# Kernel optimization log

Hardware: AMD Instinct MI355X
Metric: run time of the kernel (lower is better)

Reference implementation:

```python
import jax, jax.numpy as jnp
import numpy as np

N = 30000
E_RAND = 480000
NFEAT = 512
NHID = 64
NHEADS = 8
NCLASS = 500
ALPHA = 0.2


def setup_inputs() -> dict:
    key = jax.random.key(0)
    ks = jax.random.split(key, 8)
    features = jax.random.normal(ks[0], (N, NFEAT), dtype=jnp.float32)
    src = jax.random.randint(ks[1], (E_RAND,), 0, N, dtype=jnp.int32)
    dst = jax.random.randint(ks[2], (E_RAND,), 0, N, dtype=jnp.int32)
    loop = jnp.arange(N, dtype=jnp.int32)
    edge_index = jnp.stack([jnp.concatenate([src, loop]), jnp.concatenate([dst, loop])])  # [2, E]
    # xavier-normal-ish scaling keeps exp(-leakyrelu(.)) in a sane range
    W = jax.random.normal(ks[3], (NHEADS, NFEAT, NHID), dtype=jnp.float32) * (1.414 * np.sqrt(2.0 / (NFEAT + NHID)))
    a = jax.random.normal(ks[4], (NHEADS, 2 * NHID), dtype=jnp.float32) * (1.414 * np.sqrt(2.0 / (1 + 2 * NHID)))
    out_W = jax.random.normal(ks[5], (NHID * NHEADS, NCLASS), dtype=jnp.float32) * (1.414 * np.sqrt(2.0 / (NHID * NHEADS + NCLASS)))
    out_a = jax.random.normal(ks[6], (2 * NCLASS,), dtype=jnp.float32) * (1.414 * np.sqrt(2.0 / (1 + 2 * NCLASS)))
    return {"features": features, "edge_index": edge_index, "W": W, "a": a, "out_W": out_W, "out_a": out_a}


def _sp_gat_layer(x, W, a, src, dst, concat):
    # h = x @ W  -> [N, F']
    h = x @ W
    f = h.shape[1]
    n = x.shape[0]
    # a . cat(h[src], h[dst]) == (h @ a[:f])[src] + (h @ a[f:])[dst]  (avoids [E, 2F'] concat)
    s_src = h @ a[:f]
    s_dst = h @ a[f:]
    logits = s_src[src] + s_dst[dst]                      # [E]
    edge_e = jnp.exp(-jax.nn.leaky_relu(logits, negative_slope=ALPHA))
    # special_spmm(edge, edge_e, [N,N], ones)  -> per-row sum of attention values
    e_rowsum = jax.ops.segment_sum(edge_e, src, num_segments=n)        # [N]
    # special_spmm(edge, edge_e, [N,N], h)     -> attention-weighted neighbor sum
    h_prime = jax.ops.segment_sum(edge_e[:, None] * h[dst], src, num_segments=n)  # [N, F']
    h_prime = h_prime / e_rowsum[:, None]
    return jax.nn.elu(h_prime) if concat else h_prime


def reference(features, edge_index, W, a, out_W, out_a):
    src, dst = edge_index[0], edge_index[1]
    # multi-head sparse GAT (concat=True per head), python loop over fixed small head count
    heads = [_sp_gat_layer(features, W[i], a[i], src, dst, concat=True) for i in range(W.shape[0])]
    x = jnp.concatenate(heads, axis=1)                    # [N, nhid*nheads]
    out = jax.nn.elu(_sp_gat_layer(x, out_W, out_a, src, dst, concat=False))  # [N, nclass]
    return out
```

## Files before the change

### kernel.cpp

```cpp
#include <hip/hip_runtime.h>
#include <math.h>

typedef __attribute__((ext_vector_type(8))) short short8;
typedef __attribute__((ext_vector_type(4))) float f32x4;

#define NFEAT 512
#define HID_ALL 512
#define NCLASS 500
#define ALPHA 0.2f
#define BM 128
#define BN 128

__device__ __forceinline__ ushort f32_to_bf16(float f) {
    union { float f; unsigned u; } v; v.f = f;
    unsigned u = v.u;
    unsigned r = (u + 0x7FFFu + ((u >> 16) & 1u)) >> 16;
    return (ushort)r;
}
__device__ __forceinline__ void unpack8(uint4 u, float* f) {
    f[0] = __uint_as_float(u.x << 16);
    f[1] = __uint_as_float(u.x & 0xFFFF0000u);
    f[2] = __uint_as_float(u.y << 16);
    f[3] = __uint_as_float(u.y & 0xFFFF0000u);
    f[4] = __uint_as_float(u.z << 16);
    f[5] = __uint_as_float(u.z & 0xFFFF0000u);
    f[6] = __uint_as_float(u.w << 16);
    f[7] = __uint_as_float(u.w & 0xFFFF0000u);
}
__device__ __forceinline__ float att_w(float lg) {
    return __expf(lg > 0.f ? -lg : -ALPHA * lg);
}
__device__ __forceinline__ void gload16(const void* g, void* l) {
    __builtin_amdgcn_global_load_lds(
        (const __attribute__((address_space(1))) unsigned int*)g,
        (__attribute__((address_space(3))) unsigned int*)l,
        16, 0, 0);
}

__global__ void prep_kernel(const float* __restrict__ oa, float* __restrict__ oas,
                            float* __restrict__ oad,
                            int* __restrict__ cnt, int* __restrict__ cur,
                            float* __restrict__ s2, float* __restrict__ d2, int N) {
    int idx = blockIdx.x * blockDim.x + threadIdx.x;
    if (idx < 512) {
        oas[idx] = (idx < NCLASS) ? oa[idx] : 0.f;
        oad[idx] = (idx < NCLASS) ? oa[NCLASS + idx] : 0.f;
    }
    if (idx < N) { cnt[idx] = 0; cur[idx] = 0; s2[idx] = 0.f; d2[idx] = 0.f; }
}

__global__ __launch_bounds__(256) void transpose_w1_kernel(const float* __restrict__ W,
                                                           ushort* __restrict__ WT) {
    __shared__ float tile[64][65];
    int head = blockIdx.x >> 3;
    int f0 = (blockIdx.x & 7) << 6;
    int tx = threadIdx.x & 63, tyb = threadIdx.x >> 6;
    const float* Wh = W + ((size_t)head << 15);
#pragma unroll
    for (int r = 0; r < 16; r++) {
        int ty = (tyb << 4) + r;
        tile[ty][tx] = Wh[(size_t)(f0 + ty) * 64 + tx];
    }
    __syncthreads();
#pragma unroll
    for (int r = 0; r < 16; r++) {
        int ty = (tyb << 4) + r;
        WT[(size_t)((head << 6) + ty) * 512 + f0 + tx] = f32_to_bf16(tile[tx][ty]);
    }
}

__global__ __launch_bounds__(256) void transpose_w2_kernel(const float* __restrict__ oW,
                                                           ushort* __restrict__ WT) {
    __shared__ float tile[64][65];
    int f0 = (blockIdx.x >> 3) << 6;
    int c0 = (blockIdx.x & 7) << 6;
    int tx = threadIdx.x & 63, tyb = threadIdx.x >> 6;
#pragma unroll
    for (int r = 0; r < 16; r++) {
        int ty = (tyb << 4) + r;
        int c = c0 + tx;
        tile[ty][tx] = (c < NCLASS) ? oW[(size_t)(f0 + ty) * NCLASS + c] : 0.f;
    }
    __syncthreads();
#pragma unroll
    for (int r = 0; r < 16; r++) {
        int ty = (tyb << 4) + r;
        WT[(size_t)(c0 + ty) * 512 + f0 + tx] = f32_to_bf16(tile[tx][ty]);
    }
}

__global__ void cast_feat_kernel(const float* __restrict__ in, ushort* __restrict__ out, int n4) {
    int stride = gridDim.x * blockDim.x;
    for (int i = blockIdx.x * blockDim.x + threadIdx.x; i < n4; i += stride) {
        float4 v = reinterpret_cast<const float4*>(in)[i];
        ushort4 o;
        o.x = f32_to_bf16(v.x); o.y = f32_to_bf16(v.y);
        o.z = f32_to_bf16(v.z); o.w = f32_to_bf16(v.w);
        reinterpret_cast<ushort4*>(out)[i] = o;
    }
}

__global__ void edge_count_kernel(const int* __restrict__ src, int* __restrict__ cnt, int E) {
    int e = blockIdx.x * blockDim.x + threadIdx.x;
    if (e < E) atomicAdd(&cnt[src[e]], 1);
}

__global__ __launch_bounds__(1024) void scan_kernel(const int* __restrict__ cnt,
                                                    int* __restrict__ rowptr, int n) {
    __shared__ int part[1024];
    int t = threadIdx.x;
    int chunk = (n + 1023) >> 10;
    int beg = t * chunk;
    int end = beg + chunk; if (end > n) end = n;
    int s = 0;
    for (int i = beg; i < end; i++) s += cnt[i];
    part[t] = s;
    __syncthreads();
    for (int off = 1; off < 1024; off <<= 1) {
        int v = part[t];
        int add = (t >= off) ? part[t - off] : 0;
        __syncthreads();
        part[t] = v + add;
        __syncthreads();
    }
    int base = (t > 0) ? part[t - 1] : 0;
    for (int i = beg; i < end; i++) { rowptr[i] = base; base += cnt[i]; }
    if (t == 1023) rowptr[n] = part[1023];
}

__global__ void scatter_kernel(const int* __restrict__ src, const int* __restrict__ dst,
                               const int* __restrict__ rowptr, int* __restrict__ cur,
                               int* __restrict__ colidx, int E) {
    int e = blockIdx.x * blockDim.x + threadIdx.x;
    if (e >= E) return;
    int s = src[e];
    int p = rowptr[s] + atomicAdd(&cur[s], 1);
    colidx[p] = dst[e];
}

template <int MODE>
__global__ __launch_bounds__(256) void gemm_fused_kernel(const ushort* __restrict__ A,
                                                         const ushort* __restrict__ Bt,
                                                         ushort* __restrict__ C,
                                                         const float* __restrict__ av,
                                                         const float* __restrict__ av2,
                                                         float* __restrict__ sv,
                                                         float* __restrict__ dv,
                                                         int M) {
    __shared__ ushort As[BM * 64];
    __shared__ ushort Bs[BN * 64];
    int m0 = blockIdx.x * BM;
    int n0 = blockIdx.y * BN;
    int t = threadIdx.x;
    int lane = t & 63, wid = t >> 6;
    int wr = wid >> 1, wc = wid & 1;
    int g = lane >> 4, r15 = lane & 15;
    int srow = lane >> 3;
    int schunk = lane & 7;
    f32x4 acc[4][4] = {};
    for (int k0 = 0; k0 < 512; k0 += 64) {
        __syncthreads();
#pragma unroll
        for (int j = 0; j < 4; j++) {
            int rb = j * 32 + wid * 8;
            int r = rb + srow;
            int ca = (schunk ^ (srow & 7)) << 3;
            int rowA = m0 + r; if (rowA >= M) rowA = M - 1;
            gload16(&A[(size_t)rowA * 512 + k0 + ca], &As[rb * 64]);
            int rowB = n0 + r;
            gload16(&Bt[(size_t)rowB * 512 + k0 + ca], &Bs[rb * 64]);
        }
        __syncthreads();
#pragma unroll
        for (int kk = 0; kk < 2; kk++) {
            int coff = ((kk * 4 + g) ^ (r15 & 7)) << 3;
            short8 af[4], bfr[4];
#pragma unroll
            for (int mi = 0; mi < 4; mi++)
                af[mi] = *reinterpret_cast<const short8*>(&As[((wr << 6) + mi * 16 + r15) * 64 + coff]);
#pragma unroll
            for (int ni = 0; ni < 4; ni++)
                bfr[ni] = *reinterpret_cast<const short8*>(&Bs[((wc << 6) + ni * 16 + r15) * 64 + coff]);
#pragma unroll
            for (int mi = 0; mi < 4; mi++)
#pragma unroll
                for (int ni = 0; ni < 4; ni++)
                    acc[mi][ni] = __builtin_amdgcn_mfma_f32_16x16x32_bf16(af[mi], bfr[ni], acc[mi][ni], 0, 0, 0);
        }
    }
    int fr = g << 2;
    int col = r15;
#pragma unroll
    for (int mi = 0; mi < 4; mi++)
#pragma unroll
        for (int ni = 0; ni < 4; ni++)
#pragma unroll
            for (int r = 0; r < 4; r++) {
                int grow = m0 + (wr << 6) + mi * 16 + fr + r;
                if (grow < M) {
                    int gcol = n0 + (wc << 6) + ni * 16 + col;
                    C[(size_t)grow * 512 + gcol] = f32_to_bf16(acc[mi][ni][r]);
                }
            }
    float ws[4], wd[4];
    int h = (n0 >> 6) + wc;
#pragma unroll
    for (int ni = 0; ni < 4; ni++) {
        if (MODE == 0) {
            int k = ni * 16 + col;
            ws[ni] = av[(h << 7) + k];
            wd[ni] = av[(h << 7) + 64 + k];
        } else {
            int gcol = n0 + (wc << 6) + ni * 16 + col;
            ws[ni] = av[gcol];
            wd[ni] = av2[gcol];
        }
    }
#pragma unroll
    for (int mi = 0; mi < 4; mi++)
#pragma unroll
        for (int r = 0; r < 4; r++) {
            float ps = 0.f, pd = 0.f;
#pragma unroll
            for (int ni = 0; ni < 4; ni++) {
                float v = acc[mi][ni][r];
                ps += v * ws[ni];
                pd += v * wd[ni];
            }
#pragma unroll
            for (int off = 1; off < 16; off <<= 1) {
                ps += __shfl_xor(ps, off);
                pd += __shfl_xor(pd, off);
            }
            int grow = m0 + (wr << 6) + mi * 16 + fr + r;
            if (col == 0 && grow < M) {
                if (MODE == 0) {
                    sv[(grow << 3) + h] = ps;
                    dv[(grow << 3) + h] = pd;
                } else {
                    atomicAdd(&sv[grow], ps);
                    atomicAdd(&dv[grow], pd);
                }
            }
        }
}

#define LOAD4_1(C0,C1,C2,C3,G0,G1,G2,G3,U0,U1,U2,U3,ii)                                  \
    C0 = colidx[ii]; C1 = colidx[ii + 1]; C2 = colidx[ii + 2]; C3 = colidx[ii + 3];      \
    G0 = d1[(C0 << 3) + h]; G1 = d1[(C1 << 3) + h];                                      \
    G2 = d1[(C2 << 3) + h]; G3 = d1[(C3 << 3) + h];                                      \
    U0 = *reinterpret_cast<const uint4*>(&h1[(size_t)C0 * 512 + lane * 8]);              \
    U1 = *reinterpret_cast<const uint4*>(&h1[(size_t)C1 * 512 + lane * 8]);              \
    U2 = *reinterpret_cast<const uint4*>(&h1[(size_t)C2 * 512 + lane * 8]);              \
    U3 = *reinterpret_cast<const uint4*>(&h1[(size_t)C3 * 512 + lane * 8]);

#define CONS4(G0,G1,G2,G3,U0,U1,U2,U3)                                                   \
    {                                                                                    \
        float w0 = att_w(sn + G0), w1 = att_w(sn + G1);                                  \
        float w2 = att_w(sn + G2), w3 = att_w(sn + G3);                                  \
        rsum += (w0 + w1) + (w2 + w3);                                                   \
        float f[8];                                                                      \
        unpack8(U0, f);                                                                  \
        _Pragma("unroll") for (int q = 0; q < 8; q++) acc[q] += w0 * f[q];               \
        unpack8(U1, f);                                                                  \
        _Pragma("unroll") for (int q = 0; q < 8; q++) acc[q] += w1 * f[q];               \
        unpack8(U2, f);                                                                  \
        _Pragma("unroll") for (int q = 0; q < 8; q++) acc[q] += w2 * f[q];               \
        unpack8(U3, f);                                                                  \
        _Pragma("unroll") for (int q = 0; q < 8; q++) acc[q] += w3 * f[q];               \
    }

__global__ __launch_bounds__(256) void agg1_kernel(const ushort* __restrict__ h1,
                                                   const float* __restrict__ s1,
                                                   const float* __restrict__ d1,
                                                   const int* __restrict__ rowptr,
                                                   const int* __restrict__ colidx,
                                                   ushort* __restrict__ x, int N) {
    int lane = threadIdx.x & 63;
    int n = (blockIdx.x << 2) + (threadIdx.x >> 6);
    if (n >= N) return;
    int h = lane >> 3;
    float sn = s1[(n << 3) + h];
    float acc[8] = {0.f, 0.f, 0.f, 0.f, 0.f, 0.f, 0.f, 0.f};
    float rsum = 0.f;
    int beg = rowptr[n], end = rowptr[n + 1];
    int i = beg;
    {
        int ac0, ac1, ac2, ac3, bc0, bc1, bc2, bc3;
        float ag0, ag1, ag2, ag3, bg0, bg1, bg2, bg3;
        uint4 au0, au1, au2, au3, bu0, bu1, bu2, bu3;
        if (i + 4 <= end) {
            LOAD4_1(ac0, ac1, ac2, ac3, ag0, ag1, ag2, ag3, au0, au1, au2, au3, i);
            i += 4;
            while (i + 4 <= end) {
                LOAD4_1(bc0, bc1, bc2, bc3, bg0, bg1, bg2, bg3, bu0, bu1, bu2, bu3, i);
                i += 4;
                CONS4(ag0, ag1, ag2, ag3, au0, au1, au2, au3);
                if (i + 4 <= end) {
                    LOAD4_1(ac0, ac1, ac2, ac3, ag0, ag1, ag2, ag3, au0, au1, au2, au3, i);
                    i += 4;
                    CONS4(bg0, bg1, bg2, bg3, bu0, bu1, bu2, bu3);
                } else {
                    CONS4(bg0, bg1, bg2, bg3, bu0, bu1, bu2, bu3);
                    goto tail1;
                }
            }
            CONS4(ag0, ag1, ag2, ag3, au0, au1, au2, au3);
        }
    }
tail1:
    for (; i < end; i++) {
        int dv = colidx[i];
        float w = att_w(sn + d1[(dv << 3) + h]);
        rsum += w;
        uint4 u = *reinterpret_cast<const uint4*>(&h1[(size_t)dv * 512 + lane * 8]);
        float f[8]; unpack8(u, f);
#pragma unroll
        for (int q = 0; q < 8; q++) acc[q] += w * f[q];
    }
    float inv = 1.f / rsum;
    uint ov[4];
#pragma unroll
    for (int p = 0; p < 4; p++) {
        float v0 = acc[2 * p] * inv;     v0 = v0 > 0.f ? v0 : __expf(v0) - 1.f;
        float v1 = acc[2 * p + 1] * inv; v1 = v1 > 0.f ? v1 : __expf(v1) - 1.f;
        ov[p] = (uint)f32_to_bf16(v0) | ((uint)f32_to_bf16(v1) << 16);
    }
    uint4 o; o.x = ov[0]; o.y = ov[1]; o.z = ov[2]; o.w = ov[3];
    *reinterpret_cast<uint4*>(&x[(size_t)n * 512 + lane * 8]) = o;
}

#define LOAD4_2(C0,C1,C2,C3,G0,G1,G2,G3,U0,U1,U2,U3,ii)                                  \
    C0 = colidx[ii]; C1 = colidx[ii + 1]; C2 = colidx[ii + 2]; C3 = colidx[ii + 3];      \
    G0 = d2[C0]; G1 = d2[C1]; G2 = d2[C2]; G3 = d2[C3];                                  \
    U0 = *reinterpret_cast<const uint4*>(&h2[(size_t)C0 * 512 + c0]);                    \
    U1 = *reinterpret_cast<const uint4*>(&h2[(size_t)C1 * 512 + c0]);                    \
    U2 = *reinterpret_cast<const uint4*>(&h2[(size_t)C2 * 512 + c0]);                    \
    U3 = *reinterpret_cast<const uint4*>(&h2[(size_t)C3 * 512 + c0]);

__global__ __launch_bounds__(256) void agg2_kernel(const ushort* __restrict__ h2,
                                                   const float* __restrict__ s2,
                                                   const float* __restrict__ d2,
                                                   const int* __restrict__ rowptr,
                                                   const int* __restrict__ colidx,
                                                   float* __restrict__ out, int N) {
    int lane = threadIdx.x & 63;
    int n = (blockIdx.x << 2) + (threadIdx.x >> 6);
    if (n >= N) return;
    int c0 = lane * 8;
    float sn = s2[n];
    float acc[8] = {0.f, 0.f, 0.f, 0.f, 0.f, 0.f, 0.f, 0.f};
    float rsum = 0.f;
    int beg = rowptr[n], end = rowptr[n + 1];
    int i = beg;
    {
        int ac0, ac1, ac2, ac3, bc0, bc1, bc2, bc3;
        float ag0, ag1, ag2, ag3, bg0, bg1, bg2, bg3;
        uint4 au0, au1, au2, au3, bu0, bu1, bu2, bu3;
        if (i + 4 <= end) {
            LOAD4_2(ac0, ac1, ac2, ac3, ag0, ag1, ag2, ag3, au0, au1, au2, au3, i);
            i += 4;
            while (i + 4 <= end) {
                LOAD4_2(bc0, bc1, bc2, bc3, bg0, bg1, bg2, bg3, bu0, bu1, bu2, bu3, i);
                i += 4;
                CONS4(ag0, ag1, ag2, ag3, au0, au1, au2, au3);
                if (i + 4 <= end) {
                    LOAD4_2(ac0, ac1, ac2, ac3, ag0, ag1, ag2, ag3, au0, au1, au2, au3, i);
                    i += 4;
                    CONS4(bg0, bg1, bg2, bg3, bu0, bu1, bu2, bu3);
                } else {
                    CONS4(bg0, bg1, bg2, bg3, bu0, bu1, bu2, bu3);
                    goto tail2;
                }
            }
            CONS4(ag0, ag1, ag2, ag3, au0, au1, au2, au3);
        }
    }
tail2:
    for (; i < end; i++) {
        int dv = colidx[i];
        float w = att_w(sn + d2[dv]);
        rsum += w;
        uint4 u = *reinterpret_cast<const uint4*>(&h2[(size_t)dv * 512 + c0]);
        float f[8]; unpack8(u, f);
#pragma unroll
        for (int q = 0; q < 8; q++) acc[q] += w * f[q];
    }
    float inv = 1.f / rsum;
#pragma unroll
    for (int q = 0; q < 8; q++) {
        int c = c0 + q;
        if (c < NCLASS) {
            float v = acc[q] * inv;
            v = v > 0.f ? v : __expf(v) - 1.f;
            out[(size_t)n * NCLASS + c] = v;
        }
    }
}

extern "C" void kernel_launch(void* const* d_in, const int* in_sizes, int n_in,
                              void* d_out, int out_size, void* d_ws, size_t ws_size,
                              hipStream_t stream) {
    const float* features = (const float*)d_in[0];
    const int* edge_index = (const int*)d_in[1];
    const float* W = (const float*)d_in[2];
    const float* a = (const float*)d_in[3];
    const float* out_W = (const float*)d_in[4];
    const float* out_a = (const float*)d_in[5];
    float* out = (float*)d_out;

    int N = in_sizes[0] / NFEAT;
    int E = in_sizes[1] / 2;
    const int* src = edge_index;
    const int* dst = edge_index + E;

    char* base = (char*)d_ws;
    size_t off = 0;
    auto alloc = [&](size_t bytes) -> char* {
        char* r = base + off;
        off += (bytes + 255) & ~(size_t)255;
        return r;
    };
    ushort* featb = (ushort*)alloc((size_t)N * 512 * 2);
    ushort* h1b   = (ushort*)alloc((size_t)N * 512 * 2);
    ushort* xb    = (ushort*)alloc((size_t)N * 512 * 2);
    ushort* h2b   = featb;
    ushort* w1t   = (ushort*)alloc(512 * 512 * 2);
    ushort* w2t   = (ushort*)alloc(512 * 512 * 2);
    float* s1 = (float*)alloc((size_t)N * 8 * 4);
    float* d1 = (float*)alloc((size_t)N * 8 * 4);
    float* s2 = (float*)alloc((size_t)N * 4);
    float* d2 = (float*)alloc((size_t)N * 4);
    float* oas = (float*)alloc(512 * 4);
    float* oad = (float*)alloc(512 * 4);
    int* rowptr = (int*)alloc((size_t)(N + 1) * 4);
    int* colidx = (int*)alloc((size_t)E * 4);
    int* cnt = (int*)alloc((size_t)N * 4);
    int* cur = (int*)alloc((size_t)N * 4);
    if (off > ws_size) return;

    prep_kernel<<<(N + 255) / 256, 256, 0, stream>>>(out_a, oas, oad, cnt, cur, s2, d2, N);
    transpose_w1_kernel<<<64, 256, 0, stream>>>(W, w1t);
    transpose_w2_kernel<<<64, 256, 0, stream>>>(out_W, w2t);
    cast_feat_kernel<<<2048, 256, 0, stream>>>(features, featb, N * 512 / 4);
    edge_count_kernel<<<(E + 255) / 256, 256, 0, stream>>>(src, cnt, E);
    scan_kernel<<<1, 1024, 0, stream>>>(cnt, rowptr, N);
    scatter_kernel<<<(E + 255) / 256, 256, 0, stream>>>(src, dst, rowptr, cur, colidx, E);

    dim3 gemm_grid((N + BM - 1) / BM, HID_ALL / BN);
    gemm_fused_kernel<0><<<gemm_grid, 256, 0, stream>>>(featb, w1t, h1b, a, nullptr, s1, d1, N);
    agg1_kernel<<<(N + 3) / 4, 256, 0, stream>>>(h1b, s1, d1, rowptr, colidx, xb, N);
    gemm_fused_kernel<1><<<gemm_grid, 256, 0, stream>>>(xb, w2t, h2b, oas, oad, s2, d2, N);
    agg2_kernel<<<(N + 3) / 4, 256, 0, stream>>>(h2b, s2, d2, rowptr, colidx, out, N);
}
```

Before: 345.4 us.

## Fuse feature bf16 cast into first GEMM and merge setup kernels

The first GEMM now reads fp32 features directly and converts them to bf16 while staging into LDS, removing the separate cast kernel and its bf16 buffer. The weight transposes and the zero/prep work are merged into a single launch, and the scan's partial sums use int4 loads. This saves one full read/write pass over the features and some launch overhead. In exchange the GEMM's A tile is loaded through registers at double the byte width instead of asynchronously into LDS.

```diff
diff --git a/kernel.cpp b/kernel.cpp
--- a/kernel.cpp
+++ b/kernel.cpp
@@ -37,66 +37,58 @@
         16, 0, 0);
 }
 
-__global__ void prep_kernel(const float* __restrict__ oa, float* __restrict__ oas,
-                            float* __restrict__ oad,
-                            int* __restrict__ cnt, int* __restrict__ cur,
-                            float* __restrict__ s2, float* __restrict__ d2, int N) {
-    int idx = blockIdx.x * blockDim.x + threadIdx.x;
-    if (idx < 512) {
-        oas[idx] = (idx < NCLASS) ? oa[idx] : 0.f;
-        oad[idx] = (idx < NCLASS) ? oa[NCLASS + idx] : 0.f;
-    }
-    if (idx < N) { cnt[idx] = 0; cur[idx] = 0; s2[idx] = 0.f; d2[idx] = 0.f; }
-}
-
-__global__ __launch_bounds__(256) void transpose_w1_kernel(const float* __restrict__ W,
-                                                           ushort* __restrict__ WT) {
+__global__ __launch_bounds__(256) void setup_kernel(const float* __restrict__ W,
+                                                    ushort* __restrict__ W1T,
+                                                    const float* __restrict__ oW,
+                                                    ushort* __restrict__ W2T,
+                                                    const float* __restrict__ oa,
+                                                    float* __restrict__ oas,
+                                                    float* __restrict__ oad,
+                                                    int* __restrict__ cnt, int* __restrict__ cur,
+                                                    float* __restrict__ s2, float* __restrict__ d2,
+                                                    int N) {
     __shared__ float tile[64][65];
-    int head = blockIdx.x >> 3;
-    int f0 = (blockIdx.x & 7) << 6;
-    int tx = threadIdx.x & 63, tyb = threadIdx.x >> 6;
-    const float* Wh = W + ((size_t)head << 15);
-#pragma unroll
-    for (int r = 0; r < 16; r++) {
-        int ty = (tyb << 4) + r;
-        tile[ty][tx] = Wh[(size_t)(f0 + ty) * 64 + tx];
-    }
-    __syncthreads();
-#pragma unroll
-    for (int r = 0; r < 16; r++) {
-        int ty = (tyb << 4) + r;
-        WT[(size_t)((head << 6) + ty) * 512 + f0 + tx] = f32_to_bf16(tile[tx][ty]);
-    }
-}
-
-__global__ __launch_bounds__(256) void transpose_w2_kernel(const float* __restrict__ oW,
-                                                           ushort* __restrict__ WT) {
-    __shared__ float tile[64][65];
-    int f0 = (blockIdx.x >> 3) << 6;
-    int c0 = (blockIdx.x & 7) << 6;
-    int tx = threadIdx.x & 63, tyb = threadIdx.x >> 6;
-#pragma unroll
-    for (int r = 0; r < 16; r++) {
-        int ty = (tyb << 4) + r;
-        int c = c0 + tx;
-        tile[ty][tx] = (c < NCLASS) ? oW[(size_t)(f0 + ty) * NCLASS + c] : 0.f;
-    }
-    __syncthreads();
-#pragma unroll
-    for (int r = 0; r < 16; r++) {
-        int ty = (tyb << 4) + r;
-        WT[(size_t)(c0 + ty) * 512 + f0 + tx] = f32_to_bf16(tile[tx][ty]);
-    }
-}
-
-__global__ void cast_feat_kernel(const float* __restrict__ in, ushort* __restrict__ out, int n4) {
-    int stride = gridDim.x * blockDim.x;
-    for (int i = blockIdx.x * blockDim.x + threadIdx.x; i < n4; i += stride) {
-        float4 v = reinterpret_cast<const float4*>(in)[i];
-        ushort4 o;
-        o.x = f32_to_bf16(v.x); o.y = f32_to_bf16(v.y);
-        o.z = f32_to_bf16(v.z); o.w = f32_to_bf16(v.w);
-        reinterpret_cast<ushort4*>(out)[i] = o;
+    int bid = blockIdx.x;
+    if (bid < 64) {
+        int head = bid >> 3;
+        int f0 = (bid & 7) << 6;
+        int tx = threadIdx.x & 63, tyb = threadIdx.x >> 6;
+        const float* Wh = W + ((size_t)head << 15);
+#pragma unroll
+        for (int r = 0; r < 16; r++) {
+            int ty = (tyb << 4) + r;
+            tile[ty][tx] = Wh[(size_t)(f0 + ty) * 64 + tx];
+        }
+        __syncthreads();
+#pragma unroll
+        for (int r = 0; r < 16; r++) {
+            int ty = (tyb << 4) + r;
+            W1T[(size_t)((head << 6) + ty) * 512 + f0 + tx] = f32_to_bf16(tile[tx][ty]);
+        }
+    } else if (bid < 128) {
+        int b = bid - 64;
+        int f0 = (b >> 3) << 6;
+        int c0 = (b & 7) << 6;
+        int tx = threadIdx.x & 63, tyb = threadIdx.x >> 6;
+#pragma unroll
+        for (int r = 0; r < 16; r++) {
+            int ty = (tyb << 4) + r;
+            int c = c0 + tx;
+            tile[ty][tx] = (c < NCLASS) ? oW[(size_t)(f0 + ty) * NCLASS + c] : 0.f;
+        }
+        __syncthreads();
+#pragma unroll
+        for (int r = 0; r < 16; r++) {
+            int ty = (tyb << 4) + r;
+            W2T[(size_t)(c0 + ty) * 512 + f0 + tx] = f32_to_bf16(tile[tx][ty]);
+        }
+    } else {
+        int idx = (bid - 128) * 256 + threadIdx.x;
+        if (idx < 512) {
+            oas[idx] = (idx < NCLASS) ? oa[idx] : 0.f;
+            oad[idx] = (idx < NCLASS) ? oa[NCLASS + idx] : 0.f;
+        }
+        if (idx < N) { cnt[idx] = 0; cur[idx] = 0; s2[idx] = 0.f; d2[idx] = 0.f; }
     }
 }
 
@@ -109,11 +101,17 @@
                                                     int* __restrict__ rowptr, int n) {
     __shared__ int part[1024];
     int t = threadIdx.x;
-    int chunk = (n + 1023) >> 10;
+    int chunk = ((n + 1023) >> 10 + 0);
+    chunk = (chunk + 3) & ~3;
     int beg = t * chunk;
     int end = beg + chunk; if (end > n) end = n;
     int s = 0;
-    for (int i = beg; i < end; i++) s += cnt[i];
+    int i = beg;
+    for (; i + 4 <= end; i += 4) {
+        int4 v = *reinterpret_cast<const int4*>(&cnt[i]);
+        s += v.x + v.y + v.z + v.w;
+    }
+    for (; i < end; i++) s += cnt[i];
     part[t] = s;
     __syncthreads();
     for (int off = 1; off < 1024; off <<= 1) {
@@ -124,7 +122,7 @@
         __syncthreads();
     }
     int base = (t > 0) ? part[t - 1] : 0;
-    for (int i = beg; i < end; i++) { rowptr[i] = base; base += cnt[i]; }
+    for (i = beg; i < end; i++) { rowptr[i] = base; base += cnt[i]; }
     if (t == 1023) rowptr[n] = part[1023];
 }
 
@@ -138,8 +136,9 @@
     colidx[p] = dst[e];
 }
 
-template <int MODE>
-__global__ __launch_bounds__(256) void gemm_fused_kernel(const ushort* __restrict__ A,
+template <int MODE, int AF32>
+__global__ __launch_bounds__(256) void gemm_fused_kernel(const ushort* __restrict__ A16,
+                                                         const float* __restrict__ A32,
                                                          const ushort* __restrict__ Bt,
                                                          ushort* __restrict__ C,
                                                          const float* __restrict__ av,
@@ -164,11 +163,24 @@
         for (int j = 0; j < 4; j++) {
             int rb = j * 32 + wid * 8;
             int r = rb + srow;
-            int ca = (schunk ^ (srow & 7)) << 3;
             int rowA = m0 + r; if (rowA >= M) rowA = M - 1;
-            gload16(&A[(size_t)rowA * 512 + k0 + ca], &As[rb * 64]);
+            if (AF32) {
+                const float* srcp = &A32[(size_t)rowA * 512 + k0 + (schunk << 3)];
+                float4 p0 = *reinterpret_cast<const float4*>(srcp);
+                float4 p1 = *reinterpret_cast<const float4*>(srcp + 4);
+                short8 vv;
+                vv[0] = (short)f32_to_bf16(p0.x); vv[1] = (short)f32_to_bf16(p0.y);
+                vv[2] = (short)f32_to_bf16(p0.z); vv[3] = (short)f32_to_bf16(p0.w);
+                vv[4] = (short)f32_to_bf16(p1.x); vv[5] = (short)f32_to_bf16(p1.y);
+                vv[6] = (short)f32_to_bf16(p1.z); vv[7] = (short)f32_to_bf16(p1.w);
+                *reinterpret_cast<short8*>(&As[r * 64 + ((schunk ^ (srow & 7)) << 3)]) = vv;
+            } else {
+                int ca = (schunk ^ (srow & 7)) << 3;
+                gload16(&A16[(size_t)rowA * 512 + k0 + ca], &As[rb * 64]);
+            }
             int rowB = n0 + r;
-            gload16(&Bt[(size_t)rowB * 512 + k0 + ca], &Bs[rb * 64]);
+            int cb = (schunk ^ (srow & 7)) << 3;
+            gload16(&Bt[(size_t)rowB * 512 + k0 + cb], &Bs[rb * 64]);
         }
         __syncthreads();
 #pragma unroll
@@ -421,10 +433,9 @@
         off += (bytes + 255) & ~(size_t)255;
         return r;
     };
-    ushort* featb = (ushort*)alloc((size_t)N * 512 * 2);
     ushort* h1b   = (ushort*)alloc((size_t)N * 512 * 2);
     ushort* xb    = (ushort*)alloc((size_t)N * 512 * 2);
-    ushort* h2b   = featb;
+    ushort* h2b   = h1b;
     ushort* w1t   = (ushort*)alloc(512 * 512 * 2);
     ushort* w2t   = (ushort*)alloc(512 * 512 * 2);
     float* s1 = (float*)alloc((size_t)N * 8 * 4);
@@ -439,17 +450,18 @@
     int* cur = (int*)alloc((size_t)N * 4);
     if (off > ws_size) return;
 
-    prep_kernel<<<(N + 255) / 256, 256, 0, stream>>>(out_a, oas, oad, cnt, cur, s2, d2, N);
-    transpose_w1_kernel<<<64, 256, 0, stream>>>(W, w1t);
-    transpose_w2_kernel<<<64, 256, 0, stream>>>(out_W, w2t);
-    cast_feat_kernel<<<2048, 256, 0, stream>>>(features, featb, N * 512 / 4);
+    int zblocks = (N + 255) / 256;
+    setup_kernel<<<128 + zblocks, 256, 0, stream>>>(W, w1t, out_W, w2t, out_a, oas, oad,
+                                                    cnt, cur, s2, d2, N);
     edge_count_kernel<<<(E + 255) / 256, 256, 0, stream>>>(src, cnt, E);
     scan_kernel<<<1, 1024, 0, stream>>>(cnt, rowptr, N);
     scatter_kernel<<<(E + 255) / 256, 256, 0, stream>>>(src, dst, rowptr, cur, colidx, E);
 
     dim3 gemm_grid((N + BM - 1) / BM, HID_ALL / BN);
-    gemm_fused_kernel<0><<<gemm_grid, 256, 0, stream>>>(featb, w1t, h1b, a, nullptr, s1, d1, N);
+    gemm_fused_kernel<0, 1><<<gemm_grid, 256, 0, stream>>>(nullptr, features, w1t, h1b,
+                                                           a, nullptr, s1, d1, N);
     agg1_kernel<<<(N + 3) / 4, 256, 0, stream>>>(h1b, s1, d1, rowptr, colidx, xb, N);
-    gemm_fused_kernel<1><<<gemm_grid, 256, 0, stream>>>(xb, w2t, h2b, oas, oad, s2, d2, N);
+    gemm_fused_kernel<1, 0><<<gemm_grid, 256, 0, stream>>>(xb, nullptr, w2t, h2b,
+                                                           oas, oad, s2, d2, N);
     agg2_kernel<<<(N + 3) / 4, 256, 0, stream>>>(h2b, s2, d2, rowptr, colidx, out, N);
 }
```

Result: no change. 344.7 us (-0.2%).
